# Performance work log

Measured on AMD Instinct MI355X. Metric: run time of the kernel, lower is better.

## Reference

```python
import jax, jax.numpy as jnp
import numpy as np

B = 4096
N_DENSE = 13
N_SPARSE = 26
VOCAB = 100000
EMB = 8
CIN_SIZE = [26, 128, 128]


def setup_inputs() -> dict:
    key = jax.random.key(0)
    ks = jax.random.split(key, 24)
    s = 0.05
    dense = jax.random.normal(ks[0], (B, N_DENSE), dtype=jnp.float32)
    sparse = jax.random.randint(ks[1], (B, N_SPARSE), 0, VOCAB).astype(jnp.float32)
    inputs = jnp.concatenate([dense, sparse], axis=1)  # [B, 39]
    emb_tables = jax.random.normal(ks[2], (N_SPARSE, VOCAB, EMB), dtype=jnp.float32) * s
    linear_W = jax.random.normal(ks[3], (39, 1), dtype=jnp.float32) * s
    linear_b = jnp.zeros((1,), dtype=jnp.float32)
    # CIN Conv3d weights: kernel (H_prev, H0, 1) with out_channels H_next -> [H_next, H_prev, H0]
    W_cin0 = jax.random.normal(ks[4], (CIN_SIZE[1], CIN_SIZE[0], CIN_SIZE[0]), dtype=jnp.float32) * s
    b_cin0 = jnp.zeros((CIN_SIZE[1],), dtype=jnp.float32)
    W_cin1 = jax.random.normal(ks[5], (CIN_SIZE[2], CIN_SIZE[1], CIN_SIZE[0]), dtype=jnp.float32) * s
    b_cin1 = jnp.zeros((CIN_SIZE[2],), dtype=jnp.float32)
    cin_lin_W = jax.random.normal(ks[6], (256, 1), dtype=jnp.float32) * s
    cin_lin_b = jnp.zeros((1,), dtype=jnp.float32)
    d_W1 = jax.random.normal(ks[7], (221, 256), dtype=jnp.float32) * s
    d_b1 = jnp.zeros((256,), dtype=jnp.float32)
    d_W2 = jax.random.normal(ks[8], (256, 128), dtype=jnp.float32) * s
    d_b2 = jnp.zeros((128,), dtype=jnp.float32)
    d_W3 = jax.random.normal(ks[9], (128, 64), dtype=jnp.float32) * s
    d_b3 = jnp.zeros((64,), dtype=jnp.float32)
    d_W4 = jax.random.normal(ks[10], (64, 1), dtype=jnp.float32) * s
    d_b4 = jnp.zeros((1,), dtype=jnp.float32)
    return dict(inputs=inputs, emb_tables=emb_tables, linear_W=linear_W, linear_b=linear_b,
                W_cin0=W_cin0, b_cin0=b_cin0, W_cin1=W_cin1, b_cin1=b_cin1,
                cin_lin_W=cin_lin_W, cin_lin_b=cin_lin_b,
                d_W1=d_W1, d_b1=d_b1, d_W2=d_W2, d_b2=d_b2,
                d_W3=d_W3, d_b3=d_b3, d_W4=d_W4, d_b4=d_b4)


def reference(inputs, emb_tables, linear_W, linear_b,
              W_cin0, b_cin0, W_cin1, b_cin1, cin_lin_W, cin_lin_b,
              d_W1, d_b1, d_W2, d_b2, d_W3, d_b3, d_W4, d_b4):
    dense_in = inputs[:, :N_DENSE]                       # [B, 13]
    sparse_idx = inputs[:, N_DENSE:].astype(jnp.int32)   # [B, 26]

    # linear part over the raw inputs
    linear_out = inputs @ linear_W + linear_b            # [B, 1]

    # per-field embedding lookup: tables [F, V, E], idx [B, F] -> emb [B, F, E]
    emb = jax.vmap(lambda t, i: t[i], in_axes=(0, 1), out_axes=1)(emb_tables, sparse_idx)

    # CIN: each layer is an outer product over fields followed by a full-extent
    # Conv3d, i.e. X_{l+1}[b,o,k] = sum_{i,j} X_l[b,i,k] * X_0[b,j,k] * W[o,i,j] + b[o]
    X0 = emb
    Xi = emb
    res = []
    for W, b in ((W_cin0, b_cin0), (W_cin1, b_cin1)):
        Xi = jnp.einsum('bik,bjk,oij->bok', Xi, X0, W) + b[None, :, None]
        res.append(Xi)
    cin_feat = jnp.sum(jnp.concatenate(res, axis=1), axis=-1)  # [B, 256]
    cin_out = jax.nn.relu(cin_feat @ cin_lin_W + cin_lin_b)    # [B, 1]

    # dense MLP over [dense | flattened embeddings]
    h = jnp.concatenate([dense_in, emb.reshape(emb.shape[0], -1)], axis=1)  # [B, 221]
    h = jax.nn.relu(h @ d_W1 + d_b1)
    h = jax.nn.relu(h @ d_W2 + d_b2)
    h = jax.nn.relu(h @ d_W3 + d_b3)
    dense_out = jax.nn.relu(h @ d_W4 + d_b4)                   # [B, 1]

    return jax.nn.sigmoid(linear_out + cin_out + dense_out).reshape(-1)  # [B]
```

## Files before the change

### kernel.cpp

```cpp
#include <hip/hip_runtime.h>
#include <math.h>

#define B     4096
#define ND    13
#define NS    26
#define NF    39
#define VOCAB 100000
#define NP    351
#define NPP   360
#define CHP   45
#define GSTR  28
#define RPB   8
#define TPB   512
#define XSS   212

#define OFF_GST 0
#define OFF_CST 10080
#define OFF_C2J 10088

__global__ __launch_bounds__(256) void k_pre(const float* __restrict__ W0,
                                             const float* __restrict__ W1,
                                             const float* __restrict__ b0,
                                             const float* __restrict__ b1,
                                             const float* __restrict__ clw,
                                             float* __restrict__ Gst,
                                             float* __restrict__ cst,
                                             float* __restrict__ c2j) {
    int blk = blockIdx.x, tid = threadIdx.x;
    if (blk < 26) {
        int j = blk;
        __shared__ float vh[2][128];
        __shared__ float vj[128];
        __shared__ float c2r[2];
        {
            int i = tid & 127, h = tid >> 7;
            const float* wp = W1 + (long)(h * 64) * 3328 + i * 26 + j;
            float acc = 0.f;
#pragma unroll 8
            for (int o = 0; o < 64; o++) acc += clw[128 + h * 64 + o] * wp[o * 3328];
            vh[h][i] = acc;
        }
        __syncthreads();
        if (tid < 128) {
            float vv = vh[0][tid] + vh[1][tid];
            vj[tid] = vv;
            float c = vv * b0[tid];
            for (int off = 32; off; off >>= 1) c += __shfl_down(c, off, 64);
            if ((tid & 63) == 0) c2r[tid >> 6] = c;
        }
        __syncthreads();
        if (tid == 0) c2j[j] = c2r[0] + c2r[1];
        for (int p = tid; p < NPP; p += 256) {
            float g = 0.f;
            if (p < NP) {
                int l = 0, rem = p;
                while (rem >= NS - l) { rem -= NS - l; l++; }
                int m = l + rem;
                float sym = (l != m) ? 1.f : 0.f;
                const float* wa = W0 + l * 26 + m;
                const float* wb = W0 + m * 26 + l;
#pragma unroll 8
                for (int i = 0; i < 128; i++)
                    g += vj[i] * (wa[i * 676] + sym * wb[i * 676]);
            }
            Gst[p * GSTR + j] = g;
        }
    } else if (blk == 26) {
        for (int p = tid; p < NPP; p += 256) {
            float a = 0.f; int lmbits = 0;
            if (p < NP) {
                int l = 0, rem = p;
                while (rem >= NS - l) { rem -= NS - l; l++; }
                int m = l + rem;
                float sym = (l != m) ? 1.f : 0.f;
                const float* wa = W0 + l * 26 + m;
                const float* wb = W0 + m * 26 + l;
#pragma unroll 8
                for (int o = 0; o < 128; o++)
                    a += clw[o] * (wa[o * 676] + sym * wb[o * 676]);
                lmbits = (l << 5) | m;
            }
            Gst[p * GSTR + 26] = a;
            Gst[p * GSTR + 27] = __int_as_float(lmbits);
        }
    } else {
        __shared__ float red[2];
        float c = 0.f;
        if (tid < 128) {
            c = clw[tid] * b0[tid] + clw[128 + tid] * b1[tid];
            for (int off = 32; off; off >>= 1) c += __shfl_down(c, off, 64);
            if ((tid & 63) == 0) red[tid >> 6] = c;
        }
        __syncthreads();
        if (tid == 0) cst[0] = 8.f * (red[0] + red[1]);
    }
}

__global__ __launch_bounds__(512, 4) void k_main(
    const float* __restrict__ inputs, const float* __restrict__ tables,
    const float* __restrict__ lW, const float* __restrict__ lb,
    const float* __restrict__ Gst, const float* __restrict__ c2j,
    const float* __restrict__ cst,
    const float* __restrict__ dW1, const float* __restrict__ db1,
    const float* __restrict__ dW2, const float* __restrict__ db2,
    const float* __restrict__ dW3, const float* __restrict__ db3,
    const float* __restrict__ dW4, const float* __restrict__ db4,
    const float* __restrict__ clb,
    float* __restrict__ out) {
    __shared__ float xs[RPB][XSS];
    __shared__ float inTf[221 * 8];
    __shared__ float h1Tf[256 * 12];
    __shared__ float lin_s[RPB];
    __shared__ float redbuf[8][RPB];

    float* h2Tf = inTf;

    int tid = threadIdx.x;
    int b0r = blockIdx.x * RPB;

    if (tid < RPB * NS) {
        int r = tid / NS, f = tid - r * NS;
        int idx = (int)inputs[(b0r + r) * NF + ND + f];
        const float4* src = (const float4*)(tables + ((long)f * VOCAB + idx) * 8);
        float4 a = src[0], b4 = src[1];
        *(float4*)&xs[r][f * 8] = a;
        *(float4*)&xs[r][f * 8 + 4] = b4;
        int cb = (ND + f * 8) * 8 + r;
        inTf[cb]      = a.x;  inTf[cb + 8]   = a.y;
        inTf[cb + 16] = a.z;  inTf[cb + 24]  = a.w;
        inTf[cb + 32] = b4.x; inTf[cb + 40]  = b4.y;
        inTf[cb + 48] = b4.z; inTf[cb + 56]  = b4.w;
    } else if (tid < 208 + ND * RPB) {
        int t = tid - 208;
        int c = t >> 3, r = t & 7;
        inTf[c * 8 + r] = inputs[(b0r + r) * NF + c];
    }
    if (tid >= 496 && tid < 496 + RPB) {
        int r = tid - 496;
        float acc = lb[0];
        for (int c = 0; c < NF; c++) acc += inputs[(b0r + r) * NF + c] * lW[c];
        lin_s[r] = acc;
    }
    __syncthreads();

    {
        int w = tid >> 6;
        int wu = __builtin_amdgcn_readfirstlane(w);
        int lane = tid & 63;
        int row = lane >> 3, k = lane & 7;
        const float4* g4 = (const float4*)Gst + wu * CHP * 7;
        const float* xrow = &xs[row][0];
        float csel = (wu == 0) ? 1.f : 0.f;
        float t[27];
#pragma unroll
        for (int j = 0; j < 27; j++) t[j] = 0.f;
#pragma unroll 3
        for (int pi = 0; pi < CHP; pi++) {
            float4 g6 = g4[pi * 7 + 6];
            int lm = __float_as_int(g6.w);
            float q = xrow[(lm >> 5) * 8 + k] * xrow[(lm & 31) * 8 + k];
            float4 g0 = g4[pi * 7 + 0], g1 = g4[pi * 7 + 1];
            float4 g2 = g4[pi * 7 + 2], g3 = g4[pi * 7 + 3];
            float4 g4v = g4[pi * 7 + 4], g5 = g4[pi * 7 + 5];
            t[0]  += g0.x * q; t[1]  += g0.y * q; t[2]  += g0.z * q; t[3]  += g0.w * q;
            t[4]  += g1.x * q; t[5]  += g1.y * q; t[6]  += g1.z * q; t[7]  += g1.w * q;
            t[8]  += g2.x * q; t[9]  += g2.y * q; t[10] += g2.z * q; t[11] += g2.w * q;
            t[12] += g3.x * q; t[13] += g3.y * q; t[14] += g3.z * q; t[15] += g3.w * q;
            t[16] += g4v.x * q; t[17] += g4v.y * q; t[18] += g4v.z * q; t[19] += g4v.w * q;
            t[20] += g5.x * q; t[21] += g5.y * q; t[22] += g5.z * q; t[23] += g5.w * q;
            t[24] += g6.x * q; t[25] += g6.y * q; t[26] += g6.z * q;
        }
        float part = t[26];
#pragma unroll
        for (int j = 0; j < 26; j++) {
            float xv = xrow[j * 8 + k];
            part += (t[j] + csel * c2j[j]) * xv;
        }
        part += __shfl_xor(part, 1, 64);
        part += __shfl_xor(part, 2, 64);
        part += __shfl_xor(part, 4, 64);
        if (k == 0) redbuf[w][row] = part;
    }

    {
        int o = tid & 255, g = tid >> 8;
        const float* ip = inTf + 4 * g;
        float4 A = make_float4(0.f, 0.f, 0.f, 0.f);
#pragma unroll 4
        for (int c = 0; c < 221; c++) {
            float wv = dW1[c * 256 + o];
            float4 iv = *(const float4*)&ip[c * 8];
            A.x += iv.x * wv; A.y += iv.y * wv; A.z += iv.z * wv; A.w += iv.w * wv;
        }
        float bb = db1[o];
        float4 S;
        S.x = fmaxf(A.x + bb, 0.f); S.y = fmaxf(A.y + bb, 0.f);
        S.z = fmaxf(A.z + bb, 0.f); S.w = fmaxf(A.w + bb, 0.f);
        *(float4*)&h1Tf[o * 12 + 4 * g] = S;
    }
    __syncthreads();

    {
        int o = tid & 127, g = tid >> 7;
        const float* ip = h1Tf + 2 * g;
        float a0 = 0.f, a1 = 0.f;
#pragma unroll 4
        for (int c = 0; c < 256; c++) {
            float wv = dW2[c * 128 + o];
            float2 iv = *(const float2*)&ip[c * 12];
            a0 += iv.x * wv; a1 += iv.y * wv;
        }
        float bb = db2[o];
        a0 = fmaxf(a0 + bb, 0.f); a1 = fmaxf(a1 + bb, 0.f);
        h2Tf[o * 12 + 2 * g]     = a0;
        h2Tf[o * 12 + 2 * g + 1] = a1;
    }
    __syncthreads();

    {
        int o = tid & 63, g = tid >> 6;
        float acc = 0.f;
#pragma unroll 4
        for (int c = 0; c < 128; c++) {
            float wv = dW3[c * 64 + o];
            float hv = h2Tf[c * 12 + g];
            acc += hv * wv;
        }
        float h3 = fmaxf(acc + db3[o], 0.f) * dW4[o];
        h3 += __shfl_xor(h3, 1, 64);
        h3 += __shfl_xor(h3, 2, 64);
        h3 += __shfl_xor(h3, 4, 64);
        h3 += __shfl_xor(h3, 8, 64);
        h3 += __shfl_xor(h3, 16, 64);
        h3 += __shfl_xor(h3, 32, 64);
        if (o == 0) {
            float scin = cst[0];
#pragma unroll
            for (int w2 = 0; w2 < 8; w2++) scin += redbuf[w2][g];
            float dense = fmaxf(h3 + db4[0], 0.f);
            float cin = fmaxf(scin + clb[0], 0.f);
            float x = lin_s[g] + cin + dense;
            out[b0r + g] = 1.f / (1.f + expf(-x));
        }
    }
}

extern "C" void kernel_launch(void* const* d_in, const int* in_sizes, int n_in,
                              void* d_out, int out_size, void* d_ws, size_t ws_size,
                              hipStream_t stream) {
    const float* inputs = (const float*)d_in[0];
    const float* tables = (const float*)d_in[1];
    const float* lW     = (const float*)d_in[2];
    const float* lb     = (const float*)d_in[3];
    const float* W0     = (const float*)d_in[4];
    const float* b0     = (const float*)d_in[5];
    const float* W1c    = (const float*)d_in[6];
    const float* b1c    = (const float*)d_in[7];
    const float* clw    = (const float*)d_in[8];
    const float* clb    = (const float*)d_in[9];
    const float* dW1    = (const float*)d_in[10];
    const float* db1    = (const float*)d_in[11];
    const float* dW2    = (const float*)d_in[12];
    const float* db2    = (const float*)d_in[13];
    const float* dW3    = (const float*)d_in[14];
    const float* db3    = (const float*)d_in[15];
    const float* dW4    = (const float*)d_in[16];
    const float* db4    = (const float*)d_in[17];

    float* ws   = (float*)d_ws;
    float* Gst  = ws + OFF_GST;
    float* cst  = ws + OFF_CST;
    float* c2j  = ws + OFF_C2J;

    k_pre<<<28, 256, 0, stream>>>(W0, W1c, b0, b1c, clw, Gst, cst, c2j);
    k_main<<<B / RPB, TPB, 0, stream>>>(inputs, tables, lW, lb, Gst, c2j, cst,
                                        dW1, db1, dW2, db2, dW3, db3, dW4, db4, clb,
                                        (float*)d_out);
}
```

Baseline: 248.1 us.

## Halve rows per block and remap CIN chunks to half-waves

Cuts rows per block from 8 to 4 and threads from 512 to 256. Each half-wave now handles one CIN pair chunk for 4 rows, and the dense MLP stages are remapped to the smaller block. Embedding transposition into the MLP input buffer moves after the barrier as a strided loop, and an extra barrier separates the CIN stage from the MLP. The intent is twice as many blocks for better occupancy and latency hiding, at the cost of less weight reuse per row and more total weight reads from global memory.

Result: slower. 282.2 us (+13.7%).

```diff
diff --git a/kernel.cpp b/kernel.cpp
--- a/kernel.cpp
+++ b/kernel.cpp
@@ -10,8 +10,8 @@
 #define NPP   360
 #define CHP   45
 #define GSTR  28
-#define RPB   8
-#define TPB   512
+#define RPB   4
+#define TPB   256
 #define XSS   212
 
 #define OFF_GST 0
@@ -96,7 +96,7 @@
     }
 }
 
-__global__ __launch_bounds__(512, 4) void k_main(
+__global__ __launch_bounds__(256, 4) void k_main(
     const float* __restrict__ inputs, const float* __restrict__ tables,
     const float* __restrict__ lW, const float* __restrict__ lb,
     const float* __restrict__ Gst, const float* __restrict__ c2j,
@@ -108,12 +108,12 @@
     const float* __restrict__ clb,
     float* __restrict__ out) {
     __shared__ float xs[RPB][XSS];
-    __shared__ float inTf[221 * 8];
-    __shared__ float h1Tf[256 * 12];
+    __shared__ float inTf[221 * RPB];
+    __shared__ float h1f[256 * RPB];
     __shared__ float lin_s[RPB];
-    __shared__ float redbuf[8][RPB];
-
-    float* h2Tf = inTf;
+    __shared__ float redbuf[4][RPB];
+
+    float* h2f = inTf;
 
     int tid = threadIdx.x;
     int b0r = blockIdx.x * RPB;
@@ -125,48 +125,48 @@
         float4 a = src[0], b4 = src[1];
         *(float4*)&xs[r][f * 8] = a;
         *(float4*)&xs[r][f * 8 + 4] = b4;
-        int cb = (ND + f * 8) * 8 + r;
-        inTf[cb]      = a.x;  inTf[cb + 8]   = a.y;
-        inTf[cb + 16] = a.z;  inTf[cb + 24]  = a.w;
-        inTf[cb + 32] = b4.x; inTf[cb + 40]  = b4.y;
-        inTf[cb + 48] = b4.z; inTf[cb + 56]  = b4.w;
-    } else if (tid < 208 + ND * RPB) {
-        int t = tid - 208;
-        int c = t >> 3, r = t & 7;
-        inTf[c * 8 + r] = inputs[(b0r + r) * NF + c];
-    }
-    if (tid >= 496 && tid < 496 + RPB) {
-        int r = tid - 496;
+    } else if (tid < 104 + ND * RPB) {
+        int t = tid - 104;
+        int c = t >> 2, r = t & 3;
+        inTf[c * 4 + r] = inputs[(b0r + r) * NF + c];
+    }
+    if (tid >= 192 && tid < 192 + RPB) {
+        int r = tid - 192;
         float acc = lb[0];
         for (int c = 0; c < NF; c++) acc += inputs[(b0r + r) * NF + c] * lW[c];
         lin_s[r] = acc;
     }
     __syncthreads();
 
-    {
-        int w = tid >> 6;
-        int wu = __builtin_amdgcn_readfirstlane(w);
-        int lane = tid & 63;
-        int row = lane >> 3, k = lane & 7;
-        const float4* g4 = (const float4*)Gst + wu * CHP * 7;
+    for (int e = tid; e < 208 * RPB; e += TPB) {
+        int c13 = e >> 2, r = e & 3;
+        inTf[(ND + c13) * 4 + r] = xs[r][c13];
+    }
+    {
+        int w = tid >> 6, lane = tid & 63;
+        int pg = lane >> 5;
+        int row = (lane >> 3) & 3;
+        int k = lane & 7;
+        int chunk = w * 2 + pg;
+        const float4* grow = (const float4*)(Gst + chunk * CHP * GSTR);
         const float* xrow = &xs[row][0];
-        float csel = (wu == 0) ? 1.f : 0.f;
+        float csel = (chunk == 0) ? 1.f : 0.f;
         float t[27];
 #pragma unroll
         for (int j = 0; j < 27; j++) t[j] = 0.f;
-#pragma unroll 3
+#pragma unroll 2
         for (int pi = 0; pi < CHP; pi++) {
-            float4 g6 = g4[pi * 7 + 6];
+            float4 g6 = grow[pi * 7 + 6];
             int lm = __float_as_int(g6.w);
             float q = xrow[(lm >> 5) * 8 + k] * xrow[(lm & 31) * 8 + k];
-            float4 g0 = g4[pi * 7 + 0], g1 = g4[pi * 7 + 1];
-            float4 g2 = g4[pi * 7 + 2], g3 = g4[pi * 7 + 3];
-            float4 g4v = g4[pi * 7 + 4], g5 = g4[pi * 7 + 5];
+            float4 g0 = grow[pi * 7 + 0], g1 = grow[pi * 7 + 1];
+            float4 g2 = grow[pi * 7 + 2], g3 = grow[pi * 7 + 3];
+            float4 g4 = grow[pi * 7 + 4], g5 = grow[pi * 7 + 5];
             t[0]  += g0.x * q; t[1]  += g0.y * q; t[2]  += g0.z * q; t[3]  += g0.w * q;
             t[4]  += g1.x * q; t[5]  += g1.y * q; t[6]  += g1.z * q; t[7]  += g1.w * q;
             t[8]  += g2.x * q; t[9]  += g2.y * q; t[10] += g2.z * q; t[11] += g2.w * q;
             t[12] += g3.x * q; t[13] += g3.y * q; t[14] += g3.z * q; t[15] += g3.w * q;
-            t[16] += g4v.x * q; t[17] += g4v.y * q; t[18] += g4v.z * q; t[19] += g4v.w * q;
+            t[16] += g4.x * q; t[17] += g4.y * q; t[18] += g4.z * q; t[19] += g4.w * q;
             t[20] += g5.x * q; t[21] += g5.y * q; t[22] += g5.z * q; t[23] += g5.w * q;
             t[24] += g6.x * q; t[25] += g6.y * q; t[26] += g6.z * q;
         }
@@ -179,41 +179,41 @@
         part += __shfl_xor(part, 1, 64);
         part += __shfl_xor(part, 2, 64);
         part += __shfl_xor(part, 4, 64);
-        if (k == 0) redbuf[w][row] = part;
-    }
-
-    {
-        int o = tid & 255, g = tid >> 8;
-        const float* ip = inTf + 4 * g;
+        part += __shfl_xor(part, 32, 64);
+        if ((lane & 39) == 0) redbuf[w][row] = part;
+    }
+    __syncthreads();
+
+    {
+        int o = tid;
         float4 A = make_float4(0.f, 0.f, 0.f, 0.f);
 #pragma unroll 4
         for (int c = 0; c < 221; c++) {
             float wv = dW1[c * 256 + o];
-            float4 iv = *(const float4*)&ip[c * 8];
+            float4 iv = *(const float4*)&inTf[c * 4];
             A.x += iv.x * wv; A.y += iv.y * wv; A.z += iv.z * wv; A.w += iv.w * wv;
         }
         float bb = db1[o];
         float4 S;
         S.x = fmaxf(A.x + bb, 0.f); S.y = fmaxf(A.y + bb, 0.f);
         S.z = fmaxf(A.z + bb, 0.f); S.w = fmaxf(A.w + bb, 0.f);
-        *(float4*)&h1Tf[o * 12 + 4 * g] = S;
-    }
-    __syncthreads();
-
-    {
-        int o = tid & 127, g = tid >> 7;
-        const float* ip = h1Tf + 2 * g;
+        *(float4*)&h1f[o * 4] = S;
+    }
+    __syncthreads();
+
+    {
+        int o = tid & 127, h = tid >> 7;
         float a0 = 0.f, a1 = 0.f;
 #pragma unroll 4
         for (int c = 0; c < 256; c++) {
             float wv = dW2[c * 128 + o];
-            float2 iv = *(const float2*)&ip[c * 12];
+            float2 iv = *(const float2*)&h1f[c * 4 + 2 * h];
             a0 += iv.x * wv; a1 += iv.y * wv;
         }
         float bb = db2[o];
-        a0 = fmaxf(a0 + bb, 0.f); a1 = fmaxf(a1 + bb, 0.f);
-        h2Tf[o * 12 + 2 * g]     = a0;
-        h2Tf[o * 12 + 2 * g + 1] = a1;
+        float2 S;
+        S.x = fmaxf(a0 + bb, 0.f); S.y = fmaxf(a1 + bb, 0.f);
+        *(float2*)&h2f[o * 4 + 2 * h] = S;
     }
     __syncthreads();
 
@@ -223,7 +223,7 @@
 #pragma unroll 4
         for (int c = 0; c < 128; c++) {
             float wv = dW3[c * 64 + o];
-            float hv = h2Tf[c * 12 + g];
+            float hv = h2f[c * 4 + g];
             acc += hv * wv;
         }
         float h3 = fmaxf(acc + db3[o], 0.f) * dW4[o];
@@ -236,7 +236,7 @@
         if (o == 0) {
             float scin = cst[0];
 #pragma unroll
-            for (int w2 = 0; w2 < 8; w2++) scin += redbuf[w2][g];
+            for (int w2 = 0; w2 < 4; w2++) scin += redbuf[w2][g];
             float dense = fmaxf(h3 + db4[0], 0.f);
             float cin = fmaxf(scin + clb[0], 0.f);
             float x = lin_s[g] + cin + dense;
```
